# Performance work log

Hardware: AMD Instinct MI355X
Metric: run time of the kernel (lower is better)

## Reference

```python
import jax, jax.numpy as jnp
import numpy as np

N_VERTS = 200_000
N_FACES = 400_000
N_EDGES = 2_000_000
EPS = 1e-8


def setup_inputs() -> dict:
    key = jax.random.key(0)
    ks = jax.random.split(key, 7)
    verts = jax.random.normal(ks[0], (N_VERTS, 3), dtype=jnp.float32)
    icontour_grad = jax.random.normal(ks[1], (N_VERTS, 3), dtype=jnp.float32)
    faces = jax.random.randint(ks[2], (N_FACES, 3), 0, N_VERTS)
    nodes_from = jax.random.randint(ks[3], (N_EDGES,), 0, N_VERTS)
    faces_to = jax.random.randint(ks[4], (N_EDGES,), 0, N_FACES)
    edge_labels = jax.random.randint(ks[5], (N_EDGES,), 0, 4)
    edge_emb = jax.random.normal(ks[6], (4, 4), dtype=jnp.float32)
    return dict(verts=verts, icontour_grad=icontour_grad, faces=faces,
                nodes_from=nodes_from, faces_to=faces_to,
                edge_labels=edge_labels, edge_emb=edge_emb)


def _face_normals(verts, face_idx):
    # FaceNormals: unit normal of each gathered triangle. face_idx: [E,3]
    tri = verts[face_idx]                      # [E,3,3] gather
    n = jnp.cross(tri[:, 1] - tri[:, 0], tri[:, 2] - tri[:, 0])
    return n / (jnp.linalg.norm(n, axis=-1, keepdims=True) + EPS)


def _embed_onehot(labels, weight):
    # Faithful to Model.embed(): (W^T @ onehot(labels)^T)^T == onehot @ W
    onehot = jax.nn.one_hot(labels, weight.shape[0], dtype=weight.dtype)
    return onehot @ weight                     # [E, emb_dim]


def reference(verts, icontour_grad, faces, nodes_from, faces_to, edge_labels, edge_emb):
    # make_face2node geometry on proximity-derived edges
    edge_faces = faces[faces_to]               # [E,3]
    normals_to = _face_normals(verts, edge_faces)   # [E,3]
    nodes_to = edge_faces[:, 0]                # [E]
    relative_pos = verts[nodes_from] - verts[nodes_to]        # [E,3]
    dists_normal = jnp.sum(relative_pos * normals_to, axis=-1, keepdims=True)  # [E,1]
    node2face = dists_normal * normals_to      # [E,3]
    # node2face[dists_normal < 0] *= -1
    node2face = jnp.where(dists_normal < 0, -node2face, node2face)
    n2f_distance = jnp.abs(dists_normal)       # [E,1]
    # no enclosed-nodes mask in this example -> repulsion_sign stays +1
    repulsion_sign = jnp.ones_like(dists_normal)
    # onehot-matmul edge-type embedding (edgetype_embedding, 4 classes -> dim 4)
    edge_type_emb = _embed_onehot(edge_labels, edge_emb)       # [E,4]
    return jnp.concatenate([node2face, n2f_distance, repulsion_sign, edge_type_emb], axis=-1)  # [E,9]
```

## Files before the change

kernel.cpp:

```cpp
#include <hip/hip_runtime.h>

#define EPS 1e-8f

__device__ __forceinline__ float opaque(float x) {
    asm volatile("" : "+v"(x));
    return x;
}

__device__ __forceinline__ void face_normal_ref(
    const float* __restrict__ verts, const int* __restrict__ faces, int f,
    float& nx, float& ny, float& nz, float& v0x, float& v0y, float& v0z)
{
#pragma clang fp contract(off)
    const int i0 = faces[3 * f + 0];
    const int i1 = faces[3 * f + 1];
    const int i2 = faces[3 * f + 2];

    v0x = verts[3 * i0 + 0]; v0y = verts[3 * i0 + 1]; v0z = verts[3 * i0 + 2];
    const float v1x = verts[3 * i1 + 0], v1y = verts[3 * i1 + 1], v1z = verts[3 * i1 + 2];
    const float v2x = verts[3 * i2 + 0], v2y = verts[3 * i2 + 1], v2z = verts[3 * i2 + 2];

    const float ax = v1x - v0x, ay = v1y - v0y, az = v1z - v0z;
    const float bx = v2x - v0x, by = v2y - v0y, bz = v2z - v0z;

    const float ryz = opaque(az * by);
    const float rzx = opaque(ax * bz);
    const float rxy = opaque(ay * bx);
    nx = __builtin_fmaf(ay, bz, -ryz);
    ny = __builtin_fmaf(az, bx, -rzx);
    nz = __builtin_fmaf(ax, by, -rxy);

    const float ss    = (nx * nx + ny * ny) + nz * nz;
    const float denom = sqrtf(ss) + EPS;
    nx /= denom; ny /= denom; nz /= denom;
}

__device__ __forceinline__ void edge_tail(
    float nx, float ny, float nz, float v0x, float v0y, float v0z,
    int nfrom, int label,
    const float* __restrict__ verts, const float* emb,
    float* __restrict__ r)
{
#pragma clang fp contract(off)
    const float fx = verts[3 * nfrom + 0] - v0x;
    const float fy = verts[3 * nfrom + 1] - v0y;
    const float fz = verts[3 * nfrom + 2] - v0z;

    const float d  = (fx * nx + fy * ny) + fz * nz;
    const float ad = fabsf(d);

    r[0] = ad * nx;
    r[1] = ad * ny;
    r[2] = ad * nz;
    r[3] = ad;
    r[4] = 1.0f;
    r[5] = emb[4 * label + 0];
    r[6] = emb[4 * label + 1];
    r[7] = emb[4 * label + 2];
    r[8] = emb[4 * label + 3];
}

extern "C" __global__ __launch_bounds__(256)
void face_pre_kernel(
    const float* __restrict__ verts,
    const int*   __restrict__ faces,
    float*       __restrict__ rec,
    int n_faces)
{
    const int f = blockIdx.x * blockDim.x + threadIdx.x;
    if (f >= n_faces) return;

    float nx, ny, nz, v0x, v0y, v0z;
    face_normal_ref(verts, faces, f, nx, ny, nz, v0x, v0y, v0z);

    float4* r4 = reinterpret_cast<float4*>(rec);
    r4[2 * f + 0] = make_float4(nx, ny, nz, v0x);
    r4[2 * f + 1] = make_float4(v0y, v0z, 0.0f, 0.0f);
}

extern "C" __global__ __launch_bounds__(256)
void edges_rec_kernel(
    const float* __restrict__ verts,
    const float* __restrict__ rec,
    const int*   __restrict__ nodes_from,
    const int*   __restrict__ faces_to,
    const int*   __restrict__ edge_labels,
    const float* __restrict__ edge_emb,
    float*       __restrict__ out,
    int n_edges)
{
    __shared__ float emb[16];
    if (threadIdx.x < 16) emb[threadIdx.x] = edge_emb[threadIdx.x];
    __syncthreads();

    const float4* rec4 = reinterpret_cast<const float4*>(rec);
    const int t    = blockIdx.x * blockDim.x + threadIdx.x;
    const int base = t * 4;
    if (base >= n_edges) return;

    if (base + 3 < n_edges) {
        const int4 ft = *reinterpret_cast<const int4*>(faces_to    + base);
        const int4 nf = *reinterpret_cast<const int4*>(nodes_from  + base);
        const int4 el = *reinterpret_cast<const int4*>(edge_labels + base);

        float res[36];
        const int fs[4] = {ft.x, ft.y, ft.z, ft.w};
        const int ns[4] = {nf.x, nf.y, nf.z, nf.w};
        const int ls[4] = {el.x, el.y, el.z, el.w};
#pragma unroll
        for (int k = 0; k < 4; ++k) {
            const float4 a = rec4[2 * fs[k] + 0];
            const float4 b = rec4[2 * fs[k] + 1];
            edge_tail(a.x, a.y, a.z, a.w, b.x, b.y, ns[k], ls[k], verts, emb, res + 9 * k);
        }

        float4* __restrict__ op = reinterpret_cast<float4*>(out + (size_t)base * 9);
        const float4* rp = reinterpret_cast<const float4*>(res);
#pragma unroll
        for (int i = 0; i < 9; ++i) op[i] = rp[i];
    } else {
        for (int e = base; e < n_edges; ++e) {
            const float4 a = rec4[2 * faces_to[e] + 0];
            const float4 b = rec4[2 * faces_to[e] + 1];
            float r[9];
            edge_tail(a.x, a.y, a.z, a.w, b.x, b.y, nodes_from[e], edge_labels[e], verts, emb, r);
#pragma unroll
            for (int i = 0; i < 9; ++i) out[(size_t)e * 9 + i] = r[i];
        }
    }
}

extern "C" __global__ __launch_bounds__(256)
void edges_fallback_kernel(
    const float* __restrict__ verts,
    const int*   __restrict__ faces,
    const int*   __restrict__ nodes_from,
    const int*   __restrict__ faces_to,
    const int*   __restrict__ edge_labels,
    const float* __restrict__ edge_emb,
    float*       __restrict__ out,
    int n_edges)
{
    __shared__ float emb[16];
    if (threadIdx.x < 16) emb[threadIdx.x] = edge_emb[threadIdx.x];
    __syncthreads();

    const int t    = blockIdx.x * blockDim.x + threadIdx.x;
    const int base = t * 4;
    if (base >= n_edges) return;

    const int lim = min(base + 4, n_edges);
    float res[36];
    int cnt = 0;
    for (int e = base; e < lim; ++e, ++cnt) {
        float nx, ny, nz, v0x, v0y, v0z;
        face_normal_ref(verts, faces, faces_to[e], nx, ny, nz, v0x, v0y, v0z);
        edge_tail(nx, ny, nz, v0x, v0y, v0z, nodes_from[e], edge_labels[e],
                  verts, emb, res + 9 * cnt);
    }

    if (lim == base + 4) {
        float4* __restrict__ op = reinterpret_cast<float4*>(out + (size_t)base * 9);
        const float4* rp = reinterpret_cast<const float4*>(res);
#pragma unroll
        for (int i = 0; i < 9; ++i) op[i] = rp[i];
    } else {
        for (int k = 0; k < cnt; ++k)
            for (int i = 0; i < 9; ++i)
                out[(size_t)(base + k) * 9 + i] = res[9 * k + i];
    }
}

extern "C" void kernel_launch(void* const* d_in, const int* in_sizes, int n_in,
                              void* d_out, int out_size, void* d_ws, size_t ws_size,
                              hipStream_t stream)
{
    const float* verts       = (const float*)d_in[0];
    const int*   faces       = (const int*)  d_in[2];
    const int*   nodes_from  = (const int*)  d_in[3];
    const int*   faces_to    = (const int*)  d_in[4];
    const int*   edge_labels = (const int*)  d_in[5];
    const float* edge_emb    = (const float*)d_in[6];
    float*       out         = (float*)d_out;

    const int n_faces = in_sizes[2] / 3;
    const int n_edges = in_sizes[3];

    const int block = 256;
    const int egrid = ((n_edges + 3) / 4 + block - 1) / block;

    const size_t rec_bytes = (size_t)n_faces * 8 * sizeof(float);
    if (ws_size >= rec_bytes) {
        float* rec = (float*)d_ws;
        const int fgrid = (n_faces + block - 1) / block;
        face_pre_kernel<<<fgrid, block, 0, stream>>>(verts, faces, rec, n_faces);
        edges_rec_kernel<<<egrid, block, 0, stream>>>(
            verts, rec, nodes_from, faces_to, edge_labels, edge_emb, out, n_edges);
    } else {
        edges_fallback_kernel<<<egrid, block, 0, stream>>>(
            verts, faces, nodes_from, faces_to, edge_labels, edge_emb, out, n_edges);
    }
}
```

Before: 182.3 us.

## Pad vertices to float4 and store per-face plane constant to shrink gathers

Adds a pre-pass that copies the vertex array into padded float4 storage so each random vertex gather is one 16-byte load. The per-face record shrinks from two float4s to one by storing the plane offset n·v0 in place of v0, so the edge kernel computes the signed distance as n·v_from − c. This halves the per-edge face-record gather and makes the node gather vectorised, at the cost of an extra kernel launch, more workspace, and a change in floating-point rounding order for the distance.

```diff
diff --git a/kernel.cpp b/kernel.cpp
--- a/kernel.cpp
+++ b/kernel.cpp
@@ -7,93 +7,69 @@
     return x;
 }
 
-__device__ __forceinline__ void face_normal_ref(
-    const float* __restrict__ verts, const int* __restrict__ faces, int f,
-    float& nx, float& ny, float& nz, float& v0x, float& v0y, float& v0z)
+extern "C" __global__ __launch_bounds__(256)
+void verts_pad_kernel(const float* __restrict__ verts,
+                      float4* __restrict__ verts4, int n_verts)
+{
+    const int v = blockIdx.x * blockDim.x + threadIdx.x;
+    if (v >= n_verts) return;
+    verts4[v] = make_float4(verts[3 * v + 0], verts[3 * v + 1], verts[3 * v + 2], 0.0f);
+}
+
+extern "C" __global__ __launch_bounds__(256)
+void face_pre_kernel(
+    const float4* __restrict__ verts4,
+    const int*    __restrict__ faces,
+    float4*       __restrict__ rec,
+    int n_faces)
 {
 #pragma clang fp contract(off)
+    const int f = blockIdx.x * blockDim.x + threadIdx.x;
+    if (f >= n_faces) return;
+
     const int i0 = faces[3 * f + 0];
     const int i1 = faces[3 * f + 1];
     const int i2 = faces[3 * f + 2];
 
-    v0x = verts[3 * i0 + 0]; v0y = verts[3 * i0 + 1]; v0z = verts[3 * i0 + 2];
-    const float v1x = verts[3 * i1 + 0], v1y = verts[3 * i1 + 1], v1z = verts[3 * i1 + 2];
-    const float v2x = verts[3 * i2 + 0], v2y = verts[3 * i2 + 1], v2z = verts[3 * i2 + 2];
-
-    const float ax = v1x - v0x, ay = v1y - v0y, az = v1z - v0z;
-    const float bx = v2x - v0x, by = v2y - v0y, bz = v2z - v0z;
+    const float4 v0 = verts4[i0];
+    const float4 v1 = verts4[i1];
+    const float4 v2 = verts4[i2];
+
+    const float ax = v1.x - v0.x, ay = v1.y - v0.y, az = v1.z - v0.z;
+    const float bx = v2.x - v0.x, by = v2.y - v0.y, bz = v2.z - v0.z;
 
     const float ryz = opaque(az * by);
     const float rzx = opaque(ax * bz);
     const float rxy = opaque(ay * bx);
-    nx = __builtin_fmaf(ay, bz, -ryz);
-    ny = __builtin_fmaf(az, bx, -rzx);
-    nz = __builtin_fmaf(ax, by, -rxy);
+    float nx = __builtin_fmaf(ay, bz, -ryz);
+    float ny = __builtin_fmaf(az, bx, -rzx);
+    float nz = __builtin_fmaf(ax, by, -rxy);
 
     const float ss    = (nx * nx + ny * ny) + nz * nz;
     const float denom = sqrtf(ss) + EPS;
     nx /= denom; ny /= denom; nz /= denom;
-}
-
-__device__ __forceinline__ void edge_tail(
-    float nx, float ny, float nz, float v0x, float v0y, float v0z,
-    int nfrom, int label,
-    const float* __restrict__ verts, const float* emb,
-    float* __restrict__ r)
+
+    const float c = (nx * v0.x + ny * v0.y) + nz * v0.z;
+
+    rec[f] = make_float4(nx, ny, nz, c);
+}
+
+extern "C" __global__ __launch_bounds__(256)
+void edges_rec_kernel(
+    const float4* __restrict__ verts4,
+    const float4* __restrict__ rec,
+    const int*    __restrict__ nodes_from,
+    const int*    __restrict__ faces_to,
+    const int*    __restrict__ edge_labels,
+    const float*  __restrict__ edge_emb,
+    float*        __restrict__ out,
+    int n_edges)
 {
 #pragma clang fp contract(off)
-    const float fx = verts[3 * nfrom + 0] - v0x;
-    const float fy = verts[3 * nfrom + 1] - v0y;
-    const float fz = verts[3 * nfrom + 2] - v0z;
-
-    const float d  = (fx * nx + fy * ny) + fz * nz;
-    const float ad = fabsf(d);
-
-    r[0] = ad * nx;
-    r[1] = ad * ny;
-    r[2] = ad * nz;
-    r[3] = ad;
-    r[4] = 1.0f;
-    r[5] = emb[4 * label + 0];
-    r[6] = emb[4 * label + 1];
-    r[7] = emb[4 * label + 2];
-    r[8] = emb[4 * label + 3];
-}
-
-extern "C" __global__ __launch_bounds__(256)
-void face_pre_kernel(
-    const float* __restrict__ verts,
-    const int*   __restrict__ faces,
-    float*       __restrict__ rec,
-    int n_faces)
-{
-    const int f = blockIdx.x * blockDim.x + threadIdx.x;
-    if (f >= n_faces) return;
-
-    float nx, ny, nz, v0x, v0y, v0z;
-    face_normal_ref(verts, faces, f, nx, ny, nz, v0x, v0y, v0z);
-
-    float4* r4 = reinterpret_cast<float4*>(rec);
-    r4[2 * f + 0] = make_float4(nx, ny, nz, v0x);
-    r4[2 * f + 1] = make_float4(v0y, v0z, 0.0f, 0.0f);
-}
-
-extern "C" __global__ __launch_bounds__(256)
-void edges_rec_kernel(
-    const float* __restrict__ verts,
-    const float* __restrict__ rec,
-    const int*   __restrict__ nodes_from,
-    const int*   __restrict__ faces_to,
-    const int*   __restrict__ edge_labels,
-    const float* __restrict__ edge_emb,
-    float*       __restrict__ out,
-    int n_edges)
-{
     __shared__ float emb[16];
     if (threadIdx.x < 16) emb[threadIdx.x] = edge_emb[threadIdx.x];
     __syncthreads();
 
-    const float4* rec4 = reinterpret_cast<const float4*>(rec);
     const int t    = blockIdx.x * blockDim.x + threadIdx.x;
     const int base = t * 4;
     if (base >= n_edges) return;
@@ -109,9 +85,20 @@
         const int ls[4] = {el.x, el.y, el.z, el.w};
 #pragma unroll
         for (int k = 0; k < 4; ++k) {
-            const float4 a = rec4[2 * fs[k] + 0];
-            const float4 b = rec4[2 * fs[k] + 1];
-            edge_tail(a.x, a.y, a.z, a.w, b.x, b.y, ns[k], ls[k], verts, emb, res + 9 * k);
+            const float4 r  = rec[fs[k]];
+            const float4 vf = verts4[ns[k]];
+            const float d   = ((vf.x * r.x + vf.y * r.y) + vf.z * r.z) - r.w;
+            const float ad  = fabsf(d);
+            float* o = res + 9 * k;
+            o[0] = ad * r.x;
+            o[1] = ad * r.y;
+            o[2] = ad * r.z;
+            o[3] = ad;
+            o[4] = 1.0f;
+            o[5] = emb[4 * ls[k] + 0];
+            o[6] = emb[4 * ls[k] + 1];
+            o[7] = emb[4 * ls[k] + 2];
+            o[8] = emb[4 * ls[k] + 3];
         }
 
         float4* __restrict__ op = reinterpret_cast<float4*>(out + (size_t)base * 9);
@@ -120,12 +107,16 @@
         for (int i = 0; i < 9; ++i) op[i] = rp[i];
     } else {
         for (int e = base; e < n_edges; ++e) {
-            const float4 a = rec4[2 * faces_to[e] + 0];
-            const float4 b = rec4[2 * faces_to[e] + 1];
-            float r[9];
-            edge_tail(a.x, a.y, a.z, a.w, b.x, b.y, nodes_from[e], edge_labels[e], verts, emb, r);
-#pragma unroll
-            for (int i = 0; i < 9; ++i) out[(size_t)e * 9 + i] = r[i];
+            const float4 r  = rec[faces_to[e]];
+            const float4 vf = verts4[nodes_from[e]];
+            const float d   = ((vf.x * r.x + vf.y * r.y) + vf.z * r.z) - r.w;
+            const float ad  = fabsf(d);
+            const int   l   = edge_labels[e];
+            float* o = out + (size_t)e * 9;
+            o[0] = ad * r.x; o[1] = ad * r.y; o[2] = ad * r.z;
+            o[3] = ad; o[4] = 1.0f;
+            o[5] = emb[4 * l + 0]; o[6] = emb[4 * l + 1];
+            o[7] = emb[4 * l + 2]; o[8] = emb[4 * l + 3];
         }
     }
 }
@@ -141,34 +132,51 @@
     float*       __restrict__ out,
     int n_edges)
 {
+#pragma clang fp contract(off)
     __shared__ float emb[16];
     if (threadIdx.x < 16) emb[threadIdx.x] = edge_emb[threadIdx.x];
     __syncthreads();
 
-    const int t    = blockIdx.x * blockDim.x + threadIdx.x;
-    const int base = t * 4;
-    if (base >= n_edges) return;
-
-    const int lim = min(base + 4, n_edges);
-    float res[36];
-    int cnt = 0;
-    for (int e = base; e < lim; ++e, ++cnt) {
-        float nx, ny, nz, v0x, v0y, v0z;
-        face_normal_ref(verts, faces, faces_to[e], nx, ny, nz, v0x, v0y, v0z);
-        edge_tail(nx, ny, nz, v0x, v0y, v0z, nodes_from[e], edge_labels[e],
-                  verts, emb, res + 9 * cnt);
-    }
-
-    if (lim == base + 4) {
-        float4* __restrict__ op = reinterpret_cast<float4*>(out + (size_t)base * 9);
-        const float4* rp = reinterpret_cast<const float4*>(res);
-#pragma unroll
-        for (int i = 0; i < 9; ++i) op[i] = rp[i];
-    } else {
-        for (int k = 0; k < cnt; ++k)
-            for (int i = 0; i < 9; ++i)
-                out[(size_t)(base + k) * 9 + i] = res[9 * k + i];
-    }
+    const int e = blockIdx.x * blockDim.x + threadIdx.x;
+    if (e >= n_edges) return;
+
+    const int f  = faces_to[e];
+    const int i0 = faces[3 * f + 0];
+    const int i1 = faces[3 * f + 1];
+    const int i2 = faces[3 * f + 2];
+
+    const float v0x = verts[3 * i0 + 0], v0y = verts[3 * i0 + 1], v0z = verts[3 * i0 + 2];
+    const float v1x = verts[3 * i1 + 0], v1y = verts[3 * i1 + 1], v1z = verts[3 * i1 + 2];
+    const float v2x = verts[3 * i2 + 0], v2y = verts[3 * i2 + 1], v2z = verts[3 * i2 + 2];
+
+    const float ax = v1x - v0x, ay = v1y - v0y, az = v1z - v0z;
+    const float bx = v2x - v0x, by = v2y - v0y, bz = v2z - v0z;
+
+    const float ryz = opaque(az * by);
+    const float rzx = opaque(ax * bz);
+    const float rxy = opaque(ay * bx);
+    float nx = __builtin_fmaf(ay, bz, -ryz);
+    float ny = __builtin_fmaf(az, bx, -rzx);
+    float nz = __builtin_fmaf(ax, by, -rxy);
+
+    const float ss    = (nx * nx + ny * ny) + nz * nz;
+    const float denom = sqrtf(ss) + EPS;
+    nx /= denom; ny /= denom; nz /= denom;
+
+    const int nfv = nodes_from[e];
+    const float fx = verts[3 * nfv + 0] - v0x;
+    const float fy = verts[3 * nfv + 1] - v0y;
+    const float fz = verts[3 * nfv + 2] - v0z;
+
+    const float d  = (fx * nx + fy * ny) + fz * nz;
+    const float ad = fabsf(d);
+    const int   l  = edge_labels[e];
+
+    float* o = out + (size_t)e * 9;
+    o[0] = ad * nx; o[1] = ad * ny; o[2] = ad * nz;
+    o[3] = ad; o[4] = 1.0f;
+    o[5] = emb[4 * l + 0]; o[6] = emb[4 * l + 1];
+    o[7] = emb[4 * l + 2]; o[8] = emb[4 * l + 3];
 }
 
 extern "C" void kernel_launch(void* const* d_in, const int* in_sizes, int n_in,
@@ -183,21 +191,29 @@
     const float* edge_emb    = (const float*)d_in[6];
     float*       out         = (float*)d_out;
 
+    const int n_verts = in_sizes[0] / 3;
     const int n_faces = in_sizes[2] / 3;
     const int n_edges = in_sizes[3];
 
     const int block = 256;
     const int egrid = ((n_edges + 3) / 4 + block - 1) / block;
 
-    const size_t rec_bytes = (size_t)n_faces * 8 * sizeof(float);
-    if (ws_size >= rec_bytes) {
-        float* rec = (float*)d_ws;
+    const size_t rec_bytes = (size_t)n_faces * sizeof(float4);
+    const size_t v4_bytes  = (size_t)n_verts * sizeof(float4);
+
+    if (ws_size >= rec_bytes + v4_bytes) {
+        float4* rec    = (float4*)d_ws;
+        float4* verts4 = (float4*)((char*)d_ws + rec_bytes);
+
+        const int vgrid = (n_verts + block - 1) / block;
         const int fgrid = (n_faces + block - 1) / block;
-        face_pre_kernel<<<fgrid, block, 0, stream>>>(verts, faces, rec, n_faces);
+        verts_pad_kernel<<<vgrid, block, 0, stream>>>(verts, verts4, n_verts);
+        face_pre_kernel<<<fgrid, block, 0, stream>>>(verts4, faces, rec, n_faces);
         edges_rec_kernel<<<egrid, block, 0, stream>>>(
-            verts, rec, nodes_from, faces_to, edge_labels, edge_emb, out, n_edges);
+            verts4, rec, nodes_from, faces_to, edge_labels, edge_emb, out, n_edges);
     } else {
-        edges_fallback_kernel<<<egrid, block, 0, stream>>>(
+        const int fbgrid = (n_edges + block - 1) / block;
+        edges_fallback_kernel<<<fbgrid, block, 0, stream>>>(
             verts, faces, nodes_from, faces_to, edge_labels, edge_emb, out, n_edges);
     }
 }
```

Measured after the change: 173.5 us. 4.8% less time.
